# Optimization experiments

Hardware: AMD Instinct MI355X
Metric: run time of the kernel (lower is better)

The kernel has to match this reference:

```python
import jax, jax.numpy as jnp
import numpy as np

B, S, D, H = 4, 2048, 256, 4
HD = D // H          # head_dim = 64
SPARSITY = 0.1
NH2 = H * H          # 16, distill feature size


def _linear_params(key, out_d, in_d):
    # torch nn.Linear default init: U(-1/sqrt(in), 1/sqrt(in)) for W and b
    limit = 1.0 / np.sqrt(in_d)
    kw, kb = jax.random.split(key)
    W = jax.random.uniform(kw, (out_d, in_d), minval=-limit, maxval=limit, dtype=jnp.float32)
    b = jax.random.uniform(kb, (out_d,), minval=-limit, maxval=limit, dtype=jnp.float32)
    return W, b


def setup_inputs() -> dict:
    key = jax.random.key(0)
    ks = jax.random.split(key, 8)
    x = jax.random.normal(ks[0], (B, S, D), dtype=jnp.float32)
    Wq, bq = _linear_params(ks[1], D, D)
    Wk, bk = _linear_params(ks[2], D, D)
    Wv, bv = _linear_params(ks[3], D, D)
    Wd, bd = _linear_params(ks[4], NH2, NH2)      # distill: 16 -> 16
    Wg, bg = _linear_params(ks[5], NH2, D)        # gate: dim -> 16 (then sigmoid)
    Wgp, bgp = _linear_params(ks[6], D, NH2)      # gate_projection: 16 -> dim
    Wo, bo = _linear_params(ks[7], D, D)          # out: dim -> dim
    return dict(x=x, Wq=Wq, bq=bq, Wk=Wk, bk=bk, Wv=Wv, bv=bv,
                Wd=Wd, bd=bd, Wg=Wg, bg=bg, Wgp=Wgp, bgp=bgp, Wo=Wo, bo=bo)


def reference(x, Wq, bq, Wk, bk, Wv, bv, Wd, bd, Wg, bg, Wgp, bgp, Wo, bo):
    b, s, d = x.shape
    scale = HD ** -0.5
    # QKV projections, split into heads: [b, h, s, hd]
    Q = (x @ Wq.T + bq).reshape(b, s, H, HD).transpose(0, 2, 1, 3)
    K = (x @ Wk.T + bk).reshape(b, s, H, HD).transpose(0, 2, 1, 3)
    V = (x @ Wv.T + bv).reshape(b, s, H, HD).transpose(0, 2, 1, 3)
    scores = jnp.einsum('bhqd,bhkd->bhqk', Q, K) * scale  # [b,h,s,s]
    # per-row quantile threshold (torch.quantile linear interpolation == jnp default)
    q = 1.0 - SPARSITY  # 0.9
    thr = jnp.quantile(scores, q, axis=-1, keepdims=True)
    masked = jnp.where(scores >= thr, scores, -jnp.inf)
    probs = jax.nn.softmax(masked, axis=-1)
    att = jnp.einsum('bhqk,bhkd->bhqd', probs, V)
    att = att.transpose(0, 2, 1, 3).reshape(b, s, d)  # [b,s,dim]
    # distill: view as (-1, 16) -> Linear(16,16) -> view back
    distilled = (att.reshape(-1, NH2) @ Wd.T + bd).reshape(b, s, d)
    # gate from mean-pooled input
    g = jax.nn.sigmoid(x.mean(axis=1) @ Wg.T + bg)  # [b,16]
    g = (g @ Wgp.T + bgp)[:, None, :]               # [b,1,dim] broadcast over seq
    mixed = g * distilled + (1.0 - g) * att
    return mixed @ Wo.T + bo
```

## Files before the change

kernel.cpp:

```cpp
#include <hip/hip_runtime.h>
#include <hip/hip_bf16.h>
#include <math.h>


#define CAP 128

typedef __attribute__((ext_vector_type(8))) short short8;
typedef __attribute__((ext_vector_type(4))) float floatx4;
typedef _Float16 half8 __attribute__((ext_vector_type(8)));
typedef _Float16 half4v __attribute__((ext_vector_type(4)));
#define MFMA16(a,b,c) __builtin_amdgcn_mfma_f32_16x16x32_bf16(a,b,c,0,0,0)
#define MFMAH(a,b,c)  __builtin_amdgcn_mfma_f32_16x16x32_f16(a,b,c,0,0,0)

__device__ __forceinline__ float umt(unsigned u){
  return __uint_as_float((u & 0x80000000u) ? (u & 0x7fffffffu) : ~u);
}
__device__ __forceinline__ float wmin_f(float v){
  #pragma unroll
  for (int m=1;m<64;m<<=1) v = fminf(v, __shfl_xor(v,m,64));
  return v;
}
__device__ __forceinline__ int mbcnt64(unsigned long long m){
  return (int)__builtin_amdgcn_mbcnt_hi((unsigned)(m>>32),
         __builtin_amdgcn_mbcnt_lo((unsigned)(m & 0xffffffffull), 0u));
}
__device__ __forceinline__ short8 ldb8(const __hip_bfloat16* p){
  return *(const short8*)p;
}
__device__ __forceinline__ void cvt8(short* dh, short* dl, float4 v0, float4 v1){
  const float vv[8] = {v0.x,v0.y,v0.z,v0.w,v1.x,v1.y,v1.z,v1.w};
  short8 h8, l8;
  #pragma unroll
  for (int i=0;i<8;i++){
    const __hip_bfloat16 h = __float2bfloat16(vv[i]);
    const __hip_bfloat16 l = __float2bfloat16(vv[i] - __bfloat162float(h));
    h8[i] = *(const short*)&h;
    l8[i] = *(const short*)&l;
  }
  *(short8*)dh = h8;
  *(short8*)dl = l8;
}

#define FULLSEL(SU, PSTART, V206, V205)                                        \
  {                                                                            \
    unsigned v = (PSTART);                                                     \
    _Pragma("unroll 1")                                                        \
    for (int bit = 19; bit >= 0; --bit){                                       \
      const float cf = umt(v | (1u << bit));                                   \
      int n = 0;                                                               \
      _Pragma("unroll")                                                        \
      for (int i = 0; i < 32; i++) n += (int)__popcll(__ballot(SU[i] >= cf));  \
      if (n >= 206) v |= (1u << bit);                                          \
    }                                                                          \
    V206 = umt(v);                                                             \
    int cgt = 0; float mn = 3.0e38f;                                           \
    _Pragma("unroll")                                                          \
    for (int i = 0; i < 32; i++){                                              \
      const float u = SU[i];                                                   \
      const bool gt = (u > V206);                                              \
      cgt += (int)__popcll(__ballot(gt));                                      \
      mn = (gt && u < mn) ? u : mn;                                            \
    }                                                                          \
    mn = wmin_f(mn);                                                           \
    V205 = (cgt == 205) ? mn : V206;                                           \
  }

__global__ void xpart_kernel(const float* __restrict__ x, float* __restrict__ xpart){
  const int ch = blockIdx.x, b = blockIdx.y, t = threadIdx.x;
  const float* xp = x + ((size_t)b*2048 + (size_t)ch*16)*256 + t;
  float s = 0.f;
  #pragma unroll
  for (int i=0;i<16;i++) s += xp[(size_t)i*256];
  xpart[(size_t)(b*128+ch)*256 + t] = s;
}

__global__ void gate_kernel(const float* __restrict__ xpart,
                            const float* __restrict__ Wg, const float* __restrict__ bg,
                            const float* __restrict__ Wgp,const float* __restrict__ bgp,
                            float* __restrict__ gate_ws){
  __shared__ float xm[256];
  __shared__ float part[16][17];
  __shared__ float g16[16];
  const int t = threadIdx.x;
  const int b = blockIdx.x;
  float s = 0.f;
  for (int ch=0; ch<128; ch++) s += xpart[(size_t)(b*128+ch)*256 + t];
  xm[t] = s * (1.0f/2048.0f);
  __syncthreads();
  {
    const int j = t >> 4, dg = t & 15;
    float p = 0.f;
    #pragma unroll
    for (int d=0; d<16; d++) p = fmaf(xm[dg*16+d], Wg[j*256 + dg*16 + d], p);
    part[j][dg] = p;
  }
  __syncthreads();
  if (t < 16){
    float z = bg[t];
    #pragma unroll
    for (int g=0; g<16; g++) z += part[t][g];
    g16[t] = 1.0f/(1.0f + __expf(-z));
  }
  __syncthreads();
  float z2 = bgp[t];
  #pragma unroll
  for (int j=0;j<16;j++) z2 = fmaf(g16[j], Wgp[t*16+j], z2);
  gate_ws[b*256 + t] = z2;
}

__global__ __launch_bounds__(256) void qkv_gemm(
    const float* __restrict__ x,
    const float* __restrict__ Wq, const float* __restrict__ bq,
    const float* __restrict__ Wk, const float* __restrict__ bk,
    const float* __restrict__ Wv, const float* __restrict__ bv,
    __hip_bfloat16* __restrict__ qh, __hip_bfloat16* __restrict__ ql,
    __hip_bfloat16* __restrict__ kh, __hip_bfloat16* __restrict__ kl,
    _Float16* __restrict__ vth, _Float16* __restrict__ vtl){
  __shared__ short Ah[64][40], Al[64][40];
  __shared__ short Bh[64][40], Bl[64][40];
  const int m0 = blockIdx.x * 64;
  const int n0g = blockIdx.y * 64;
  const int sect = n0g >> 8;
  const int nl0 = n0g & 255;
  const float* W    = (sect==0) ? Wq : ((sect==1) ? Wk : Wv);
  const float* bias = (sect==0) ? bq : ((sect==1) ? bk : bv);
  const int tid = threadIdx.x;
  const int lr = tid >> 2, lc = tid & 3;
  const int w = tid >> 6, ln = tid & 63;
  const int lm = ln & 15, lk = (ln >> 4) * 8;

  floatx4 acc[4];
  #pragma unroll
  for (int tl=0;tl<4;tl++) acc[tl] = (floatx4){0.f,0.f,0.f,0.f};

  for (int k0 = 0; k0 < 256; k0 += 32){
    const float4 a0 = *(const float4*)&x[(size_t)(m0 +lr)*256 + k0 + lc*8];
    const float4 a1 = *(const float4*)&x[(size_t)(m0 +lr)*256 + k0 + lc*8 + 4];
    const float4 b0 = *(const float4*)&W[(size_t)(nl0+lr)*256 + k0 + lc*8];
    const float4 b1 = *(const float4*)&W[(size_t)(nl0+lr)*256 + k0 + lc*8 + 4];
    __syncthreads();
    cvt8(&Ah[lr][lc*8], &Al[lr][lc*8], a0, a1);
    cvt8(&Bh[lr][lc*8], &Bl[lr][lc*8], b0, b1);
    __syncthreads();
    const short8 ah8 = *(const short8*)&Ah[w*16+lm][lk];
    const short8 al8 = *(const short8*)&Al[w*16+lm][lk];
    #pragma unroll
    for (int tl = 0; tl < 4; tl++){
      const short8 bh8 = *(const short8*)&Bh[tl*16+lm][lk];
      const short8 bl8 = *(const short8*)&Bl[tl*16+lm][lk];
      acc[tl] = MFMA16(ah8, bh8, acc[tl]);
      acc[tl] = MFMA16(al8, bh8, acc[tl]);
      acc[tl] = MFMA16(ah8, bl8, acc[tl]);
      acc[tl] = MFMA16(al8, bl8, acc[tl]);
    }
  }

  #pragma unroll
  for (int tl = 0; tl < 4; tl++){
    const int f = nl0 + tl*16 + lm;
    const int hh = f >> 6, hd = f & 63;
    const float bf = bias[f];
    if (sect == 2){
      const int mB = m0 + w*16 + (ln >> 4)*4;
      const int bidx = mB >> 11, s0 = mB & 2047;
      half4v hv, lv;
      #pragma unroll
      for (int i=0;i<4;i++){
        const float val = acc[tl][i] + bf;
        const _Float16 hx = (_Float16)val;
        hv[i] = hx;
        lv[i] = (_Float16)(val - (float)hx);
      }
      const size_t row = (size_t)((bidx*4+hh)*64 + hd);
      *(half4v*)(vth + row*2048 + s0) = hv;
      *(half4v*)(vtl + row*2048 + s0) = lv;
    } else {
      #pragma unroll
      for (int i=0;i<4;i++){
        const int m = m0 + w*16 + (ln >> 4)*4 + i;
        const int bidx = m >> 11, s = m & 2047;
        const float val = acc[tl][i] + bf;
        const size_t idx = (size_t)((bidx*4+hh)*2048 + s)*64 + hd;
        const __hip_bfloat16 hi = __float2bfloat16(val);
        const float lo = val - __bfloat162float(hi);
        if (sect == 0){ qh[idx] = hi; ql[idx] = __float2bfloat16(lo); }
        else          { kh[idx] = hi; kl[idx] = __float2bfloat16(lo); }
      }
    }
  }
}

__global__ __launch_bounds__(512, 4) void attn_kernel(
    const __hip_bfloat16* __restrict__ qh, const __hip_bfloat16* __restrict__ ql,
    const __hip_bfloat16* __restrict__ kh, const __hip_bfloat16* __restrict__ kl,
    const _Float16* __restrict__ vth, const _Float16* __restrict__ vtl,
    const float* __restrict__ Wd, const float* __restrict__ bd,
    const float* __restrict__ gate_ws, float* __restrict__ mix_ws){
  __shared__ __align__(16) char smem[37312];
  float (*buf)[516] = (float (*)[516])smem;
  float (*obuf)[66] = (float (*)[66])(smem + 33024);
  float* zbuf = (float*)(smem + 37248);

  const int bh = blockIdx.y;
  const int q0 = blockIdx.x * 16;
  const int tid = threadIdx.x;
  const int w = tid >> 6, ln = tid & 63;
  const int lm = ln & 15;
  const int lk = (ln >> 4) * 8;
  const int qa = 2*w, qb = 2*w + 1;

  const __hip_bfloat16* Qh = qh + ((size_t)bh*2048 + q0)*64;
  const __hip_bfloat16* Ql = ql + ((size_t)bh*2048 + q0)*64;
  const __hip_bfloat16* Kh = kh + ((size_t)bh*2048 + w*256)*64;
  const __hip_bfloat16* Kl = kl + ((size_t)bh*2048 + w*256)*64;

  float su0[32], su1[32];

  const short8 ah0 = ldb8(Qh + lm*64 + lk);
  const short8 ah1 = ldb8(Qh + lm*64 + 32 + lk);
  const short8 al0 = ldb8(Ql + lm*64 + lk);
  const short8 al1 = ldb8(Ql + lm*64 + 32 + lk);

  #pragma unroll
  for (int c = 0; c < 4; c++){
    floatx4 acc[4];
    #pragma unroll
    for (int tl = 0; tl < 4; tl++){
      const int krow = c*64 + tl*16 + lm;
      short8 bh0 = ldb8(Kh + krow*64 + lk);
      short8 bh1 = ldb8(Kh + krow*64 + 32 + lk);
      short8 bl0 = ldb8(Kl + krow*64 + lk);
      short8 bl1 = ldb8(Kl + krow*64 + 32 + lk);
      floatx4 a = {0.f,0.f,0.f,0.f};
      a = MFMA16(ah0, bh0, a);
      a = MFMA16(ah1, bh1, a);
      a = MFMA16(al0, bh0, a);
      a = MFMA16(al1, bh1, a);
      a = MFMA16(ah0, bl0, a);
      a = MFMA16(ah1, bl1, a);
      a = MFMA16(al0, bl0, a);
      a = MFMA16(al1, bl1, a);
      acc[tl] = a;
    }
    __syncthreads();
    const int wr = (ln >> 4) * 4;
    #pragma unroll
    for (int tl = 0; tl < 4; tl++){
      const int col = w*64 + tl*16 + lm;
      buf[wr+0][col] = acc[tl].x * 0.125f;
      buf[wr+1][col] = acc[tl].y * 0.125f;
      buf[wr+2][col] = acc[tl].z * 0.125f;
      buf[wr+3][col] = acc[tl].w * 0.125f;
    }
    __syncthreads();
    float4 ra0 = *(const float4*)&buf[qa][4*ln];
    float4 ra1 = *(const float4*)&buf[qa][256 + 4*ln];
    float4 rb0 = *(const float4*)&buf[qb][4*ln];
    float4 rb1 = *(const float4*)&buf[qb][256 + 4*ln];
    const int o = c*8;
    su0[o+0]=ra0.x; su0[o+1]=ra0.y; su0[o+2]=ra0.z; su0[o+3]=ra0.w;
    su0[o+4]=ra1.x; su0[o+5]=ra1.y; su0[o+6]=ra1.z; su0[o+7]=ra1.w;
    su1[o+0]=rb0.x; su1[o+1]=rb0.y; su1[o+2]=rb0.z; su1[o+3]=rb0.w;
    su1[o+4]=rb1.x; su1[o+5]=rb1.y; su1[o+6]=rb1.z; su1[o+7]=rb1.w;
  }
  __syncthreads();

  unsigned p0 = 0, p1 = 0;
  #pragma unroll 1
  for (int bit = 31; bit >= 20; --bit){
    const float c0f = umt(p0 | (1u << bit));
    const float c1f = umt(p1 | (1u << bit));
    int v0 = 0, n1 = 0;
    #pragma unroll
    for (int i = 0; i < 32; i++){
      v0 += (su0[i] >= c0f) ? 1 : 0;
      n1 += (int)__popcll(__ballot(su1[i] >= c1f));
    }
    #pragma unroll
    for (int m=1;m<64;m<<=1) v0 += __shfl_xor(v0,m,64);
    p0 |= (v0 >= 206) ? (1u << bit) : 0u;
    if (n1 >= 206) p1 |= (1u << bit);
  }

  const int b = bh >> 2, h = bh & 3;

  const float pf0  = umt(p0),             pf1  = umt(p1);
  const float hif0 = umt(p0 + 0x100000u), hif1 = umt(p1 + 0x100000u);
  float* cand0 = (float*)(smem + (size_t)w*1024);
  float* cand1 = (float*)(smem + (size_t)w*1024 + 512);

  int above0 = 0, nc0 = 0, above1 = 0, nc1 = 0;
  float mx0 = -3.0e38f, mx1 = -3.0e38f, mnab0 = 3.0e38f, mnab1 = 3.0e38f;
  #pragma unroll
  for (int i = 0; i < 32; i++){
    const float u0 = su0[i], u1 = su1[i];
    mx0 = fmaxf(mx0, u0);
    mx1 = fmaxf(mx1, u1);
    const bool ab0 = (u0 >= hif0), ab1 = (u1 >= hif1);
    above0 += ab0 ? 1 : 0;
    above1 += ab1 ? 1 : 0;
    if (ab0) mnab0 = fminf(mnab0, u0);
    if (ab1) mnab1 = fminf(mnab1, u1);
    const bool cd0 = (u0 >= pf0) && !ab0, cd1 = (u1 >= pf1) && !ab1;
    const unsigned long long bal0 = __ballot(cd0);
    if (cd0){
      const int pos = nc0 + mbcnt64(bal0);
      if (pos < CAP) cand0[pos] = u0;
    }
    nc0 += (int)__popcll(bal0);
    const unsigned long long bal1 = __ballot(cd1);
    if (cd1){
      const int pos = nc1 + mbcnt64(bal1);
      if (pos < CAP) cand1[pos] = u1;
    }
    nc1 += (int)__popcll(bal1);
  }
  int ab01 = above0 | (above1 << 16);
  #pragma unroll
  for (int m=1;m<64;m<<=1){
    ab01  += __shfl_xor(ab01, m,64);
    mx0   = fmaxf(mx0,   __shfl_xor(mx0,  m,64));
    mx1   = fmaxf(mx1,   __shfl_xor(mx1,  m,64));
    mnab0 = fminf(mnab0, __shfl_xor(mnab0,m,64));
    mnab1 = fminf(mnab1, __shfl_xor(mnab1,m,64));
  }
  above0 = ab01 & 0xffff;
  above1 = ab01 >> 16;

  float v206_0, v205_0, v206_1, v205_1;
  if (__builtin_expect(nc0 <= CAP && nc1 <= CAP, 1)){
    const int j0 = 206 - above0, j1 = 206 - above1;
    const float cv00 = (ln      < nc0) ? cand0[ln]      : -3.0e38f;
    const float cv01 = (ln + 64 < nc0) ? cand0[ln + 64] : -3.0e38f;
    const float cv10 = (ln      < nc1) ? cand1[ln]      : -3.0e38f;
    const float cv11 = (ln + 64 < nc1) ? cand1[ln + 64] : -3.0e38f;
    unsigned v0 = p0, v1 = p1;
    #pragma unroll 1
    for (int bit = 19; bit >= 0; --bit){
      const float cf0 = umt(v0 | (1u << bit));
      const float cf1 = umt(v1 | (1u << bit));
      const int n0 = (int)__popcll(__ballot(cv00 >= cf0))
                   + (int)__popcll(__ballot(cv01 >= cf0));
      const int n1 = (int)__popcll(__ballot(cv10 >= cf1))
                   + (int)__popcll(__ballot(cv11 >= cf1));
      if (n0 >= j0) v0 |= (1u << bit);
      if (n1 >= j1) v1 |= (1u << bit);
    }
    v206_0 = umt(v0);
    v206_1 = umt(v1);
    const int cgtc0 = (int)__popcll(__ballot(cv00 > v206_0))
                    + (int)__popcll(__ballot(cv01 > v206_0));
    const int cgtc1 = (int)__popcll(__ballot(cv10 > v206_1))
                    + (int)__popcll(__ballot(cv11 > v206_1));
    float mnc0 = 3.0e38f, mnc1 = 3.0e38f;
    if (cv00 > v206_0) mnc0 = fminf(mnc0, cv00);
    if (cv01 > v206_0) mnc0 = fminf(mnc0, cv01);
    if (cv10 > v206_1) mnc1 = fminf(mnc1, cv10);
    if (cv11 > v206_1) mnc1 = fminf(mnc1, cv11);
    #pragma unroll
    for (int m=1;m<64;m<<=1){
      mnc0 = fminf(mnc0, __shfl_xor(mnc0,m,64));
      mnc1 = fminf(mnc1, __shfl_xor(mnc1,m,64));
    }
    const int cgt0 = above0 + cgtc0, cgt1 = above1 + cgtc1;
    v205_0 = (cgt0 == 205) ? ((cgtc0 > 0) ? mnc0 : mnab0) : v206_0;
    v205_1 = (cgt1 == 205) ? ((cgtc1 > 0) ? mnc1 : mnab1) : v206_1;
  } else {
    FULLSEL(su0, p0, v206_0, v205_0);
    FULLSEL(su1, p1, v206_1, v205_1);
  }

  const float thr0 = (float)((double)v206_0 + 0.3*((double)v205_0 - (double)v206_0));
  const float thr1 = (float)((double)v206_1 + 0.3*((double)v205_1 - (double)v206_1));

  __syncthreads();

  float zl0 = 0.f, zl1 = 0.f;
  char* rba = smem + (size_t)qa*2048 + ((size_t)(ln >> 4) << 9)
            + (size_t)((((ln & 15) << 3)) ^ ((qa & 7) << 4));
  char* rbb = smem + (size_t)qb*2048 + ((size_t)(ln >> 4) << 9)
            + (size_t)((((ln & 15) << 3)) ^ ((qb & 7) << 4));

  const int ct = w & 3, khq = w >> 2;
  const int arow = ln & 15;
  const int sw = (arow & 7) << 4;
  const char* prow = smem + (size_t)arow*2048;
  const int klog0 = (khq << 10) + ((ln >> 4) << 4);
  floatx4 acch = {0.f,0.f,0.f,0.f};
  floatx4 accl = {0.f,0.f,0.f,0.f};

  #pragma unroll
  for (int hp = 0; hp < 2; hp++){
    #pragma unroll
    for (int c = 0; c < 4; c++){
      half4v pk0, pk1;
      #pragma unroll
      for (int jj = 0; jj < 4; jj++){
        const int i = c*8 + hp*4 + jj;
        const float s0 = su0[i], s1 = su1[i];
        const float pr0 = (s0 >= thr0) ? __expf(s0 - mx0) : 0.f;
        const float pr1 = (s1 >= thr1) ? __expf(s1 - mx1) : 0.f;
        const _Float16 ph0 = (_Float16)pr0;
        const _Float16 ph1 = (_Float16)pr1;
        zl0 += (float)ph0;
        zl1 += (float)ph1;
        pk0[jj] = ph0;
        pk1[jj] = ph1;
      }
      *(half4v*)(rba + c*128) = pk0;
      *(half4v*)(rbb + c*128) = pk1;
    }
    if (hp == 1){
      #pragma unroll
      for (int m=1;m<64;m<<=1){
        zl0 += __shfl_xor(zl0,m,64);
        zl1 += __shfl_xor(zl1,m,64);
      }
      if (ln == 0){ zbuf[qa] = 1.0f / zl0; zbuf[qb] = 1.0f / zl1; }
    }
    __syncthreads();

    const _Float16* vhp_ = vth + ((size_t)bh*64 + ct*16 + arow)*2048
                         + (hp << 10) + (khq << 9) + ((ln >> 4) << 3);
    const _Float16* vlp_ = vtl + ((size_t)bh*64 + ct*16 + arow)*2048
                         + (hp << 10) + (khq << 9) + ((ln >> 4) << 3);
    #pragma unroll 4
    for (int kk = 0; kk < 16; kk++){
      const half8 a   = *(const half8*)(prow + ((klog0 + kk*64) ^ sw));
      const half8 vh8 = *(const half8*)(vhp_ + kk*32);
      const half8 vl8 = *(const half8*)(vlp_ + kk*32);
      acch = MFMAH(a, vh8, acch);
      accl = MFMAH(a, vl8, accl);
    }
    if (hp == 0) __syncthreads();
  }
  floatx4 acc = acch + accl;

  float gt = 0.f, bda = 0.f;
  float wdv[16];
  if (khq == 1){
    const int r0 = (ln >> 4) * 4;
    #pragma unroll
    for (int i = 0; i < 4; i++) obuf[r0+i][ct*16 + arow] = acc[i];
  } else {
    gt  = gate_ws[(size_t)b*256 + h*64 + ct*16 + arow];
    bda = bd[arow];
    #pragma unroll
    for (int m4 = 0; m4 < 4; m4++){
      const float4 t4 = *(const float4*)&Wd[arow*16 + m4*4];
      wdv[m4*4+0]=t4.x; wdv[m4*4+1]=t4.y; wdv[m4*4+2]=t4.z; wdv[m4*4+3]=t4.w;
    }
  }
  __syncthreads();
  if (khq == 0){
    const int r0 = (ln >> 4) * 4;
    const int gb = ln & 48;
    #pragma unroll
    for (int i = 0; i < 4; i++){
      const int r = r0 + i;
      const float o = (acc[i] + obuf[r][ct*16 + arow]) * zbuf[r];
      float d = bda;
      #pragma unroll
      for (int m = 0; m < 16; m++)
        d = fmaf(__shfl(o, gb + m, 64), wdv[m], d);
      const float mixed = gt*d + (1.0f - gt)*o;
      mix_ws[(size_t)(b*2048 + q0 + r)*256 + h*64 + ct*16 + arow] = mixed;
    }
  }
}

__global__ __launch_bounds__(256) void out_gemm(
    const float* __restrict__ A, const float* __restrict__ Wo,
    const float* __restrict__ bo, float* __restrict__ out){
  __shared__ short Ah[64][40], Al[64][40];
  __shared__ short Bh[64][40], Bl[64][40];
  const int m0 = blockIdx.x * 64;
  const int n0 = blockIdx.y * 64;
  const int tid = threadIdx.x;
  const int lr = tid >> 2, lc = tid & 3;
  const int w = tid >> 6, ln = tid & 63;
  const int lm = ln & 15, lk = (ln >> 4) * 8;

  floatx4 acc[4];
  #pragma unroll
  for (int tl=0;tl<4;tl++) acc[tl] = (floatx4){0.f,0.f,0.f,0.f};

  for (int k0 = 0; k0 < 256; k0 += 32){
    const float4 a0 = *(const float4*)&A [(size_t)(m0+lr)*256 + k0 + lc*8];
    const float4 a1 = *(const float4*)&A [(size_t)(m0+lr)*256 + k0 + lc*8 + 4];
    const float4 b0 = *(const float4*)&Wo[(size_t)(n0+lr)*256 + k0 + lc*8];
    const float4 b1 = *(const float4*)&Wo[(size_t)(n0+lr)*256 + k0 + lc*8 + 4];
    __syncthreads();
    cvt8(&Ah[lr][lc*8], &Al[lr][lc*8], a0, a1);
    cvt8(&Bh[lr][lc*8], &Bl[lr][lc*8], b0, b1);
    __syncthreads();
    const short8 ah8 = *(const short8*)&Ah[w*16+lm][lk];
    const short8 al8 = *(const short8*)&Al[w*16+lm][lk];
    #pragma unroll
    for (int tl = 0; tl < 4; tl++){
      const short8 bh8 = *(const short8*)&Bh[tl*16+lm][lk];
      const short8 bl8 = *(const short8*)&Bl[tl*16+lm][lk];
      acc[tl] = MFMA16(ah8, bh8, acc[tl]);
      acc[tl] = MFMA16(al8, bh8, acc[tl]);
      acc[tl] = MFMA16(ah8, bl8, acc[tl]);
      acc[tl] = MFMA16(al8, bl8, acc[tl]);
    }
  }

  #pragma unroll
  for (int tl = 0; tl < 4; tl++){
    const int f = n0 + tl*16 + lm;
    const float bf = bo[f];
    #pragma unroll
    for (int i=0;i<4;i++){
      const int m = m0 + w*16 + (ln >> 4)*4 + i;
      out[(size_t)m*256 + f] = acc[tl][i] + bf;
    }
  }
}

extern "C" void kernel_launch(void* const* d_in, const int* in_sizes, int n_in,
                              void* d_out, int out_size, void* d_ws, size_t ws_size,
                              hipStream_t stream) {
  const float* x   = (const float*)d_in[0];
  const float* Wq  = (const float*)d_in[1];  const float* bq  = (const float*)d_in[2];
  const float* Wk  = (const float*)d_in[3];  const float* bk  = (const float*)d_in[4];
  const float* Wv  = (const float*)d_in[5];  const float* bv  = (const float*)d_in[6];
  const float* Wd  = (const float*)d_in[7];  const float* bd  = (const float*)d_in[8];
  const float* Wg  = (const float*)d_in[9];  const float* bg  = (const float*)d_in[10];
  const float* Wgp = (const float*)d_in[11]; const float* bgp = (const float*)d_in[12];
  const float* Wo  = (const float*)d_in[13]; const float* bo  = (const float*)d_in[14];

  char* base = (char*)d_ws;
  float* mix_ws = (float*)(base);
  __hip_bfloat16* qh = (__hip_bfloat16*)(base + (size_t)( 8<<20));
  __hip_bfloat16* ql = (__hip_bfloat16*)(base + (size_t)(12<<20));
  __hip_bfloat16* kh = (__hip_bfloat16*)(base + (size_t)(16<<20));
  __hip_bfloat16* kl = (__hip_bfloat16*)(base + (size_t)(20<<20));
  _Float16* vth = (_Float16*)(base + (size_t)(24<<20));
  _Float16* vtl = (_Float16*)(base + (size_t)(28<<20));
  float* xpart  = (float*)(base + (size_t)(32<<20));
  float* gate_ws= (float*)(base + (size_t)(33<<20));

  xpart_kernel<<<dim3(128,4), 256, 0, stream>>>(x, xpart);
  gate_kernel<<<4, 256, 0, stream>>>(xpart, Wg, bg, Wgp, bgp, gate_ws);
  qkv_gemm<<<dim3(128,12), 256, 0, stream>>>(x, Wq,bq, Wk,bk, Wv,bv,
                                             qh, ql, kh, kl, vth, vtl);
  attn_kernel<<<dim3(128,16), 512, 0, stream>>>(qh, ql, kh, kl, vth, vtl,
                                                Wd, bd, gate_ws, mix_ws);
  out_gemm<<<dim3(128,4), 256, 0, stream>>>(mix_ws, Wo, bo, (float*)d_out);
}
```

Before: 405.8 us.

## Pre-split activations and weights into bf16 hi/lo once; double-buffer attention score smem

x is split into bf16 hi/lo pairs inside the existing xpart pass, and a new kernel splits Wq/Wk/Wv/Wo once, so neither GEMM converts in its inner loop anymore. The attention kernel writes its mixed output directly as hi/lo bf16 for the output GEMM. The attention kernel also double-buffers its score staging buffer, which removes two __syncthreads, at the cost of roughly doubling its shared memory, which may reduce occupancy. The cost is one extra launch and extra workspace traffic for the pre-split copies.

```diff
diff --git a/kernel.cpp b/kernel.cpp
--- a/kernel.cpp
+++ b/kernel.cpp
@@ -26,19 +26,6 @@
 }
 __device__ __forceinline__ short8 ldb8(const __hip_bfloat16* p){
   return *(const short8*)p;
-}
-__device__ __forceinline__ void cvt8(short* dh, short* dl, float4 v0, float4 v1){
-  const float vv[8] = {v0.x,v0.y,v0.z,v0.w,v1.x,v1.y,v1.z,v1.w};
-  short8 h8, l8;
-  #pragma unroll
-  for (int i=0;i<8;i++){
-    const __hip_bfloat16 h = __float2bfloat16(vv[i]);
-    const __hip_bfloat16 l = __float2bfloat16(vv[i] - __bfloat162float(h));
-    h8[i] = *(const short*)&h;
-    l8[i] = *(const short*)&l;
-  }
-  *(short8*)dh = h8;
-  *(short8*)dl = l8;
 }
 
 #define FULLSEL(SU, PSTART, V206, V205)                                        \
@@ -65,13 +52,40 @@
     V205 = (cgt == 205) ? mn : V206;                                           \
   }
 
-__global__ void xpart_kernel(const float* __restrict__ x, float* __restrict__ xpart){
+__global__ void xpart_kernel(const float* __restrict__ x, float* __restrict__ xpart,
+                             __hip_bfloat16* __restrict__ xh, __hip_bfloat16* __restrict__ xl){
   const int ch = blockIdx.x, b = blockIdx.y, t = threadIdx.x;
-  const float* xp = x + ((size_t)b*2048 + (size_t)ch*16)*256 + t;
+  const size_t base = ((size_t)b*2048 + (size_t)ch*16)*256 + t;
   float s = 0.f;
   #pragma unroll
-  for (int i=0;i<16;i++) s += xp[(size_t)i*256];
+  for (int i=0;i<16;i++){
+    const float v = x[base + (size_t)i*256];
+    s += v;
+    const __hip_bfloat16 h = __float2bfloat16(v);
+    xh[base + (size_t)i*256] = h;
+    xl[base + (size_t)i*256] = __float2bfloat16(v - __bfloat162float(h));
+  }
   xpart[(size_t)(b*128+ch)*256 + t] = s;
+}
+
+__global__ void wconv_kernel(const float* __restrict__ Wq, const float* __restrict__ Wk,
+                             const float* __restrict__ Wv, const float* __restrict__ Wo,
+                             __hip_bfloat16* __restrict__ wh, __hip_bfloat16* __restrict__ wl){
+  const int mat = blockIdx.x >> 6;
+  const float* W = (mat==0) ? Wq : (mat==1) ? Wk : (mat==2) ? Wv : Wo;
+  const int off = (blockIdx.x & 63)*1024 + threadIdx.x*4;
+  const float4 v = *(const float4*)&W[off];
+  const float vv[4] = {v.x, v.y, v.z, v.w};
+  short hs[4], ls[4];
+  #pragma unroll
+  for (int i=0;i<4;i++){
+    const __hip_bfloat16 h = __float2bfloat16(vv[i]);
+    const __hip_bfloat16 l = __float2bfloat16(vv[i] - __bfloat162float(h));
+    hs[i] = *(const short*)&h; ls[i] = *(const short*)&l;
+  }
+  const size_t o = (size_t)mat*65536 + off;
+  *(short4*)((short*)wh + o) = make_short4(hs[0],hs[1],hs[2],hs[3]);
+  *(short4*)((short*)wl + o) = make_short4(ls[0],ls[1],ls[2],ls[3]);
 }
 
 __global__ void gate_kernel(const float* __restrict__ xpart,
@@ -109,10 +123,9 @@
 }
 
 __global__ __launch_bounds__(256) void qkv_gemm(
-    const float* __restrict__ x,
-    const float* __restrict__ Wq, const float* __restrict__ bq,
-    const float* __restrict__ Wk, const float* __restrict__ bk,
-    const float* __restrict__ Wv, const float* __restrict__ bv,
+    const __hip_bfloat16* __restrict__ xh, const __hip_bfloat16* __restrict__ xl,
+    const __hip_bfloat16* __restrict__ wh, const __hip_bfloat16* __restrict__ wl,
+    const float* __restrict__ bq, const float* __restrict__ bk, const float* __restrict__ bv,
     __hip_bfloat16* __restrict__ qh, __hip_bfloat16* __restrict__ ql,
     __hip_bfloat16* __restrict__ kh, __hip_bfloat16* __restrict__ kl,
     _Float16* __restrict__ vth, _Float16* __restrict__ vtl){
@@ -122,7 +135,8 @@
   const int n0g = blockIdx.y * 64;
   const int sect = n0g >> 8;
   const int nl0 = n0g & 255;
-  const float* W    = (sect==0) ? Wq : ((sect==1) ? Wk : Wv);
+  const __hip_bfloat16* Wh = wh + (size_t)sect*65536;
+  const __hip_bfloat16* Wl = wl + (size_t)sect*65536;
   const float* bias = (sect==0) ? bq : ((sect==1) ? bk : bv);
   const int tid = threadIdx.x;
   const int lr = tid >> 2, lc = tid & 3;
@@ -134,13 +148,15 @@
   for (int tl=0;tl<4;tl++) acc[tl] = (floatx4){0.f,0.f,0.f,0.f};
 
   for (int k0 = 0; k0 < 256; k0 += 32){
-    const float4 a0 = *(const float4*)&x[(size_t)(m0 +lr)*256 + k0 + lc*8];
-    const float4 a1 = *(const float4*)&x[(size_t)(m0 +lr)*256 + k0 + lc*8 + 4];
-    const float4 b0 = *(const float4*)&W[(size_t)(nl0+lr)*256 + k0 + lc*8];
-    const float4 b1 = *(const float4*)&W[(size_t)(nl0+lr)*256 + k0 + lc*8 + 4];
+    const short8 a_h = ldb8(xh + (size_t)(m0 +lr)*256 + k0 + lc*8);
+    const short8 a_l = ldb8(xl + (size_t)(m0 +lr)*256 + k0 + lc*8);
+    const short8 b_h = ldb8(Wh + (size_t)(nl0+lr)*256 + k0 + lc*8);
+    const short8 b_l = ldb8(Wl + (size_t)(nl0+lr)*256 + k0 + lc*8);
     __syncthreads();
-    cvt8(&Ah[lr][lc*8], &Al[lr][lc*8], a0, a1);
-    cvt8(&Bh[lr][lc*8], &Bl[lr][lc*8], b0, b1);
+    *(short8*)&Ah[lr][lc*8] = a_h;
+    *(short8*)&Al[lr][lc*8] = a_l;
+    *(short8*)&Bh[lr][lc*8] = b_h;
+    *(short8*)&Bl[lr][lc*8] = b_l;
     __syncthreads();
     const short8 ah8 = *(const short8*)&Ah[w*16+lm][lk];
     const short8 al8 = *(const short8*)&Al[w*16+lm][lk];
@@ -195,11 +211,13 @@
     const __hip_bfloat16* __restrict__ kh, const __hip_bfloat16* __restrict__ kl,
     const _Float16* __restrict__ vth, const _Float16* __restrict__ vtl,
     const float* __restrict__ Wd, const float* __restrict__ bd,
-    const float* __restrict__ gate_ws, float* __restrict__ mix_ws){
-  __shared__ __align__(16) char smem[37312];
-  float (*buf)[516] = (float (*)[516])smem;
-  float (*obuf)[66] = (float (*)[66])(smem + 33024);
-  float* zbuf = (float*)(smem + 37248);
+    const float* __restrict__ gate_ws,
+    __hip_bfloat16* __restrict__ mixh, __hip_bfloat16* __restrict__ mixl){
+  __shared__ __align__(16) char smem[70336];
+  float (*buf0)[516] = (float (*)[516])smem;
+  float (*buf1)[516] = (float (*)[516])(smem + 33024);
+  float (*obuf)[66] = (float (*)[66])(smem + 66048);
+  float* zbuf = (float*)(smem + 70272);
 
   const int bh = blockIdx.y;
   const int q0 = blockIdx.x * 16;
@@ -223,6 +241,7 @@
 
   #pragma unroll
   for (int c = 0; c < 4; c++){
+    float (*bufc)[516] = (c & 1) ? buf1 : buf0;
     floatx4 acc[4];
     #pragma unroll
     for (int tl = 0; tl < 4; tl++){
@@ -242,21 +261,20 @@
       a = MFMA16(al1, bl1, a);
       acc[tl] = a;
     }
-    __syncthreads();
     const int wr = (ln >> 4) * 4;
     #pragma unroll
     for (int tl = 0; tl < 4; tl++){
       const int col = w*64 + tl*16 + lm;
-      buf[wr+0][col] = acc[tl].x * 0.125f;
-      buf[wr+1][col] = acc[tl].y * 0.125f;
-      buf[wr+2][col] = acc[tl].z * 0.125f;
-      buf[wr+3][col] = acc[tl].w * 0.125f;
+      bufc[wr+0][col] = acc[tl].x * 0.125f;
+      bufc[wr+1][col] = acc[tl].y * 0.125f;
+      bufc[wr+2][col] = acc[tl].z * 0.125f;
+      bufc[wr+3][col] = acc[tl].w * 0.125f;
     }
     __syncthreads();
-    float4 ra0 = *(const float4*)&buf[qa][4*ln];
-    float4 ra1 = *(const float4*)&buf[qa][256 + 4*ln];
-    float4 rb0 = *(const float4*)&buf[qb][4*ln];
-    float4 rb1 = *(const float4*)&buf[qb][256 + 4*ln];
+    float4 ra0 = *(const float4*)&bufc[qa][4*ln];
+    float4 ra1 = *(const float4*)&bufc[qa][256 + 4*ln];
+    float4 rb0 = *(const float4*)&bufc[qb][4*ln];
+    float4 rb1 = *(const float4*)&bufc[qb][256 + 4*ln];
     const int o = c*8;
     su0[o+0]=ra0.x; su0[o+1]=ra0.y; su0[o+2]=ra0.z; su0[o+3]=ra0.w;
     su0[o+4]=ra1.x; su0[o+5]=ra1.y; su0[o+6]=ra1.z; su0[o+7]=ra1.w;
@@ -286,8 +304,8 @@
 
   const float pf0  = umt(p0),             pf1  = umt(p1);
   const float hif0 = umt(p0 + 0x100000u), hif1 = umt(p1 + 0x100000u);
-  float* cand0 = (float*)(smem + (size_t)w*1024);
-  float* cand1 = (float*)(smem + (size_t)w*1024 + 512);
+  float* cand0 = (float*)(smem + 33024 + (size_t)w*1024);
+  float* cand1 = (float*)(smem + 33024 + (size_t)w*1024 + 512);
 
   int above0 = 0, nc0 = 0, above1 = 0, nc1 = 0;
   float mx0 = -3.0e38f, mx1 = -3.0e38f, mnab0 = 3.0e38f, mnab1 = 3.0e38f;
@@ -373,8 +391,6 @@
   const float thr0 = (float)((double)v206_0 + 0.3*((double)v205_0 - (double)v206_0));
   const float thr1 = (float)((double)v206_1 + 0.3*((double)v205_1 - (double)v206_1));
 
-  __syncthreads();
-
   float zl0 = 0.f, zl1 = 0.f;
   char* rba = smem + (size_t)qa*2048 + ((size_t)(ln >> 4) << 9)
             + (size_t)((((ln & 15) << 3)) ^ ((qa & 7) << 4));
@@ -464,18 +480,24 @@
       for (int m = 0; m < 16; m++)
         d = fmaf(__shfl(o, gb + m, 64), wdv[m], d);
       const float mixed = gt*d + (1.0f - gt)*o;
-      mix_ws[(size_t)(b*2048 + q0 + r)*256 + h*64 + ct*16 + arow] = mixed;
+      const size_t oidx = (size_t)(b*2048 + q0 + r)*256 + h*64 + ct*16 + arow;
+      const __hip_bfloat16 mhv = __float2bfloat16(mixed);
+      mixh[oidx] = mhv;
+      mixl[oidx] = __float2bfloat16(mixed - __bfloat162float(mhv));
     }
   }
 }
 
 __global__ __launch_bounds__(256) void out_gemm(
-    const float* __restrict__ A, const float* __restrict__ Wo,
+    const __hip_bfloat16* __restrict__ mh, const __hip_bfloat16* __restrict__ ml,
+    const __hip_bfloat16* __restrict__ wh, const __hip_bfloat16* __restrict__ wl,
     const float* __restrict__ bo, float* __restrict__ out){
   __shared__ short Ah[64][40], Al[64][40];
   __shared__ short Bh[64][40], Bl[64][40];
   const int m0 = blockIdx.x * 64;
   const int n0 = blockIdx.y * 64;
+  const __hip_bfloat16* Wh = wh + (size_t)3*65536;
+  const __hip_bfloat16* Wl = wl + (size_t)3*65536;
   const int tid = threadIdx.x;
   const int lr = tid >> 2, lc = tid & 3;
   const int w = tid >> 6, ln = tid & 63;
@@ -486,13 +508,15 @@
   for (int tl=0;tl<4;tl++) acc[tl] = (floatx4){0.f,0.f,0.f,0.f};
 
   for (int k0 = 0; k0 < 256; k0 += 32){
-    const float4 a0 = *(const float4*)&A [(size_t)(m0+lr)*256 + k0 + lc*8];
-    const float4 a1 = *(const float4*)&A [(size_t)(m0+lr)*256 + k0 + lc*8 + 4];
-    const float4 b0 = *(const float4*)&Wo[(size_t)(n0+lr)*256 + k0 + lc*8];
-    const float4 b1 = *(const float4*)&Wo[(size_t)(n0+lr)*256 + k0 + lc*8 + 4];
+    const short8 a_h = ldb8(mh + (size_t)(m0+lr)*256 + k0 + lc*8);
+    const short8 a_l = ldb8(ml + (size_t)(m0+lr)*256 + k0 + lc*8);
+    const short8 b_h = ldb8(Wh + (size_t)(n0+lr)*256 + k0 + lc*8);
+    const short8 b_l = ldb8(Wl + (size_t)(n0+lr)*256 + k0 + lc*8);
     __syncthreads();
-    cvt8(&Ah[lr][lc*8], &Al[lr][lc*8], a0, a1);
-    cvt8(&Bh[lr][lc*8], &Bl[lr][lc*8], b0, b1);
+    *(short8*)&Ah[lr][lc*8] = a_h;
+    *(short8*)&Al[lr][lc*8] = a_l;
+    *(short8*)&Bh[lr][lc*8] = b_h;
+    *(short8*)&Bl[lr][lc*8] = b_l;
     __syncthreads();
     const short8 ah8 = *(const short8*)&Ah[w*16+lm][lk];
     const short8 al8 = *(const short8*)&Al[w*16+lm][lk];
@@ -532,21 +556,27 @@
   const float* Wo  = (const float*)d_in[13]; const float* bo  = (const float*)d_in[14];
 
   char* base = (char*)d_ws;
-  float* mix_ws = (float*)(base);
+  __hip_bfloat16* mixh = (__hip_bfloat16*)(base);
+  __hip_bfloat16* mixl = (__hip_bfloat16*)(base + (size_t)( 4<<20));
   __hip_bfloat16* qh = (__hip_bfloat16*)(base + (size_t)( 8<<20));
   __hip_bfloat16* ql = (__hip_bfloat16*)(base + (size_t)(12<<20));
   __hip_bfloat16* kh = (__hip_bfloat16*)(base + (size_t)(16<<20));
   __hip_bfloat16* kl = (__hip_bfloat16*)(base + (size_t)(20<<20));
   _Float16* vth = (_Float16*)(base + (size_t)(24<<20));
   _Float16* vtl = (_Float16*)(base + (size_t)(28<<20));
-  float* xpart  = (float*)(base + (size_t)(32<<20));
-  float* gate_ws= (float*)(base + (size_t)(33<<20));
-
-  xpart_kernel<<<dim3(128,4), 256, 0, stream>>>(x, xpart);
+  __hip_bfloat16* xh = (__hip_bfloat16*)(base + (size_t)(32<<20));
+  __hip_bfloat16* xl = (__hip_bfloat16*)(base + (size_t)(36<<20));
+  __hip_bfloat16* wh = (__hip_bfloat16*)(base + (size_t)(40<<20));
+  __hip_bfloat16* wl = (__hip_bfloat16*)(base + (size_t)(40<<20) + (512<<10));
+  float* xpart  = (float*)(base + (size_t)(41<<20));
+  float* gate_ws= (float*)(base + (size_t)(41<<20) + (512<<10));
+
+  xpart_kernel<<<dim3(128,4), 256, 0, stream>>>(x, xpart, xh, xl);
+  wconv_kernel<<<256, 256, 0, stream>>>(Wq, Wk, Wv, Wo, wh, wl);
   gate_kernel<<<4, 256, 0, stream>>>(xpart, Wg, bg, Wgp, bgp, gate_ws);
-  qkv_gemm<<<dim3(128,12), 256, 0, stream>>>(x, Wq,bq, Wk,bk, Wv,bv,
+  qkv_gemm<<<dim3(128,12), 256, 0, stream>>>(xh, xl, wh, wl, bq, bk, bv,
                                              qh, ql, kh, kl, vth, vtl);
   attn_kernel<<<dim3(128,16), 512, 0, stream>>>(qh, ql, kh, kl, vth, vtl,
-                                                Wd, bd, gate_ws, mix_ws);
-  out_gemm<<<dim3(128,4), 256, 0, stream>>>(mix_ws, Wo, bo, (float*)d_out);
-}
+                                                Wd, bd, gate_ws, mixh, mixl);
+  out_gemm<<<dim3(128,4), 256, 0, stream>>>(mixh, mixl, wh, wl, bo, (float*)d_out);
+}
```

Result: faster. 397.0 us (-2.2%).
